# Kernel optimization log

Hardware: AMD Instinct MI355X
Metric: run time of the kernel (lower is better)

## Reference

```python
import jax, jax.numpy as jnp
import numpy as np

K = 1024       # num_embeddings
D = 64         # embedding_dim
DECAY = 0.99
COMMIT = 0.25
EPS = 1e-05


def setup_inputs() -> dict:
    key = jax.random.key(0)
    k1, k2, k3 = jax.random.split(key, 3)
    x = jax.random.normal(k1, (16, 64, 64, 64), jnp.float32)  # NCHW, C == D
    embedding_weight = jax.random.normal(k2, (K, D), jnp.float32)
    ema_weight = jax.random.normal(k3, (K, D), jnp.float32)
    ema_cluster_size = jnp.zeros((K,), jnp.float32)
    return {"x": x, "embedding_weight": embedding_weight,
            "ema_cluster_size": ema_cluster_size, "ema_weight": ema_weight}


def reference(x, embedding_weight, ema_cluster_size, ema_weight):
    # NCHW -> NHWC, flatten tokens
    xp = jnp.transpose(x, (0, 2, 3, 1))            # [B,H,W,D]
    flat = xp.reshape(-1, D)                        # [N,D]
    dists = ((flat ** 2).sum(1, keepdims=True)
             + (embedding_weight ** 2).sum(1)
             - 2.0 * flat @ embedding_weight.T)     # [N,K]
    idx = jnp.argmin(dists, axis=1)                 # [N]
    encodings = jax.nn.one_hot(idx, K, dtype=flat.dtype)  # [N,K]
    quantized = jnp.take(embedding_weight, idx, axis=0).reshape(xp.shape)
    # training-mode EMA updates (scatter-add instead of dense one-hot matmuls)
    counts = jnp.zeros((K,), flat.dtype).at[idx].add(1.0)
    new_cs = ema_cluster_size * DECAY + (1.0 - DECAY) * counts
    n = new_cs.sum()
    new_cs = (new_cs + EPS) / (n + K * EPS) * n     # Laplace smoothing
    dw = jnp.zeros((K, D), flat.dtype).at[idx].add(flat)
    new_ema_weight = ema_weight * DECAY + (1.0 - DECAY) * dw
    new_embedding = new_ema_weight / new_cs[:, None]
    # commitment loss and straight-through estimator
    e_latent_loss = jnp.mean((jax.lax.stop_gradient(quantized) - xp) ** 2)
    loss = COMMIT * e_latent_loss
    q_st = xp + jax.lax.stop_gradient(quantized - xp)
    return (loss, jnp.transpose(q_st, (0, 3, 1, 2)), encodings,
            new_embedding, new_cs, new_ema_weight)
```

## Files before the change

kernel.cpp:

```cpp
#include <hip/hip_runtime.h>

#define HW 4096
#define DECAYF 0.99f
#define ONEMF 0.01f
#define EPSF 1e-5f

typedef __bf16 bf16x8 __attribute__((ext_vector_type(8)));
typedef float f32x4 __attribute__((ext_vector_type(4)));
typedef unsigned short ushort8 __attribute__((ext_vector_type(8)));

#define WS_COUNTS 65536
#define WS_NCHALF 66560
#define WS_SSE    67584
#define WS_EHI    67600
#define WS_ELO    100368

__device__ __forceinline__ float wave_reduce_add(float v) {
#pragma unroll
    for (int o = 32; o > 0; o >>= 1) v += __shfl_xor(v, o, 64);
    return v;
}

__device__ __forceinline__ unsigned short bf_rne(float f) {
    unsigned int u = __float_as_uint(f);
    unsigned int r = u + 0x7fffu + ((u >> 16) & 1u);
    return (unsigned short)(r >> 16);
}

__global__ __launch_bounds__(256) void prep_kernel(const float* __restrict__ E,
                                                   float* __restrict__ ws) {
    const int bid = blockIdx.x, tid = threadIdx.x;
    const int id = bid * 256 + tid;
    ws[id] = 0.0f;
    if (bid < 4) ws[WS_COUNTS + bid * 256 + tid] = 0.0f;
    if (bid == 4 && tid == 0) ws[WS_SSE] = 0.0f;
    const float v = E[id];
    const unsigned short h = bf_rne(v);
    const float hf = __uint_as_float((unsigned int)h << 16);
    const unsigned short l = bf_rne(v - hf);
    ((unsigned short*)(ws + WS_EHI))[id] = h;
    ((unsigned short*)(ws + WS_ELO))[id] = l;
    const int lane = tid & 63;
    const float s = wave_reduce_add(v * v);
    if (lane == 0) ws[WS_NCHALF + (id >> 6)] = -0.5f * s;
}

__global__ __launch_bounds__(256) void vq_main(const float* __restrict__ x,
                                               const float* __restrict__ E,
                                               float* __restrict__ out,
                                               float* __restrict__ ws) {
    const int tid = threadIdx.x;
    const int lane = tid & 63;
    const int w = tid >> 6;
    const int blk = blockIdx.x;
    const int b = blk >> 5;
    const int hw0 = (blk & 31) << 7;
    const int tok0 = blk << 7;

    __shared__ float xs[128 * 68];
    __shared__ int i1sh[128], i2sh[128], idx_sh[128];

    {
        const float* xb = x + ((size_t)b << 18) + hw0;
#pragma unroll
        for (int cc = 0; cc < 32; ++cc) {
            const int id = cc * 256 + tid;
            const int c = id >> 7, t = id & 127;
            xs[t * 68 + c] = xb[((size_t)c << 12) + t];
        }
    }
    __syncthreads();

    const int q = lane >> 4, m = lane & 15;

    bf16x8 Ah[2][2], Al[2][2];
#pragma unroll
    for (int t = 0; t < 2; ++t) {
        const int tok = w * 32 + t * 16 + m;
#pragma unroll
        for (int s = 0; s < 2; ++s) {
            const float* p = &xs[tok * 68 + s * 32 + q * 8];
            ushort8 hu, lu;
#pragma unroll
            for (int j = 0; j < 8; ++j) {
                const float f = p[j];
                const unsigned short h = bf_rne(f);
                const float hf = __uint_as_float((unsigned int)h << 16);
                hu[j] = h;
                lu[j] = bf_rne(f - hf);
            }
            Ah[t][s] = __builtin_bit_cast(bf16x8, hu);
            Al[t][s] = __builtin_bit_cast(bf16x8, lu);
        }
    }

    const ushort8* __restrict__ Ehp = (const ushort8*)(ws + WS_EHI);
    const ushort8* __restrict__ Elp = (const ushort8*)(ws + WS_ELO);
    const float* __restrict__ ncp = ws + WS_NCHALF;

    float b1[2][4], b2[2][4];
    int i1[2][4], i2[2][4];
#pragma unroll
    for (int t = 0; t < 2; ++t)
#pragma unroll
        for (int r = 0; r < 4; ++r) { b1[t][r] = -1e30f; b2[t][r] = -1e30f; i1[t][r] = 0; i2[t][r] = 1; }

    ushort8 nb0h = Ehp[m * 8 + q];
    ushort8 nb1h = Ehp[m * 8 + 4 + q];
    ushort8 nb0l = Elp[m * 8 + q];
    ushort8 nb1l = Elp[m * 8 + 4 + q];
    float nnc = ncp[m];

    for (int ck = 0; ck < 64; ++ck) {
        const ushort8 c0h = nb0h, c1h = nb1h, c0l = nb0l, c1l = nb1l;
        const float nc = nnc;
        if (ck < 63) {
            const int code = (ck + 1) * 16 + m;
            nb0h = Ehp[code * 8 + q];
            nb1h = Ehp[code * 8 + 4 + q];
            nb0l = Elp[code * 8 + q];
            nb1l = Elp[code * 8 + 4 + q];
            nnc = ncp[code];
        }
        const bf16x8 bh0 = __builtin_bit_cast(bf16x8, c0h);
        const bf16x8 bh1 = __builtin_bit_cast(bf16x8, c1h);
        const bf16x8 bl0 = __builtin_bit_cast(bf16x8, c0l);
        const bf16x8 bl1 = __builtin_bit_cast(bf16x8, c1l);
        const int idx = ck * 16 + m;
#pragma unroll
        for (int t = 0; t < 2; ++t) {
            f32x4 acc = {nc, nc, nc, nc};
            acc = __builtin_amdgcn_mfma_f32_16x16x32_bf16(Ah[t][0], bh0, acc, 0, 0, 0);
            acc = __builtin_amdgcn_mfma_f32_16x16x32_bf16(Ah[t][1], bh1, acc, 0, 0, 0);
            acc = __builtin_amdgcn_mfma_f32_16x16x32_bf16(Al[t][0], bh0, acc, 0, 0, 0);
            acc = __builtin_amdgcn_mfma_f32_16x16x32_bf16(Al[t][1], bh1, acc, 0, 0, 0);
            acc = __builtin_amdgcn_mfma_f32_16x16x32_bf16(Ah[t][0], bl0, acc, 0, 0, 0);
            acc = __builtin_amdgcn_mfma_f32_16x16x32_bf16(Ah[t][1], bl1, acc, 0, 0, 0);
#pragma unroll
            for (int r = 0; r < 4; ++r) {
                const float s = acc[r];
                const bool cA = s > b1[t][r];
                const bool cB = s > b2[t][r];
                b2[t][r] = cA ? b1[t][r] : (cB ? s : b2[t][r]);
                i2[t][r] = cA ? i1[t][r] : (cB ? idx : i2[t][r]);
                b1[t][r] = cA ? s : b1[t][r];
                i1[t][r] = cA ? idx : i1[t][r];
            }
        }
    }

#pragma unroll
    for (int d = 1; d < 16; d <<= 1) {
#pragma unroll
        for (int t = 0; t < 2; ++t)
#pragma unroll
            for (int r = 0; r < 4; ++r) {
                const float ob1 = __shfl_xor(b1[t][r], d, 64);
                const int   oi1 = __shfl_xor(i1[t][r], d, 64);
                const float ob2 = __shfl_xor(b2[t][r], d, 64);
                const int   oi2 = __shfl_xor(i2[t][r], d, 64);
                const bool wv = ob1 > b1[t][r];
                const float t1 = wv ? ob1 : b1[t][r]; const int ti1 = wv ? oi1 : i1[t][r];
                const float sA = wv ? b1[t][r] : ob1; const int siA = wv ? i1[t][r] : oi1;
                const float sB = wv ? ob2 : b2[t][r]; const int siB = wv ? oi2 : i2[t][r];
                const bool w2 = sB > sA;
                b1[t][r] = t1; i1[t][r] = ti1;
                b2[t][r] = w2 ? sB : sA; i2[t][r] = w2 ? siB : siA;
            }
    }
    if (m == 0) {
#pragma unroll
        for (int t = 0; t < 2; ++t)
#pragma unroll
            for (int r = 0; r < 4; ++r) {
                const int tokL = w * 32 + t * 16 + q * 4 + r;
                i1sh[tokL] = i1[t][r];
                i2sh[tokL] = i2[t][r];
            }
    }

    float dval = 0.0f;
    if (lane < 32) {
        const int tokL = w * 32 + lane;
        const int I1 = i1sh[tokL], I2 = i2sh[tokL];
        const int ca = I1 < I2 ? I1 : I2;
        const int cb = I1 < I2 ? I2 : I1;
        const float* Ea = E + ca * 64;
        const float* Eb = E + cb * 64;
        const float* xr = &xs[tokL * 68];
        double sa = 0, ea = 0, sb = 0, eb = 0, x2 = 0;
#pragma unroll 8
        for (int c = 0; c < 64; ++c) {
            const double xv = (double)xr[c];
            const double va = (double)Ea[c], vb = (double)Eb[c];
            sa += xv * va; ea += va * va;
            sb += xv * vb; eb += vb * vb;
            x2 += xv * xv;
        }
        const double qa = ea - 2.0 * sa;
        const double qb = eb - 2.0 * sb;
        int best; double qq;
        if (qb < qa) { best = cb; qq = qb; } else { best = ca; qq = qa; }
        idx_sh[tokL] = best;
        float dd = (float)(qq + x2);
        dval = dd < 0.f ? 0.f : dd;
        atomicAdd(&ws[WS_COUNTS + best], 1.0f);
    }
    const float ssum = wave_reduce_add(dval);
    if (lane == 0) atomicAdd(&ws[WS_SSE], ssum);
    __syncthreads();

    float* outq = out + 1;
#pragma unroll
    for (int cc = 0; cc < 32; ++cc) {
        const int id = cc * 256 + tid;
        const int c = id >> 7, t = id & 127;
        const int kb = idx_sh[t];
        const float xv = xs[t * 68 + c];
        const float eq = E[kb * 64 + c];
        outq[((size_t)(b * 64 + c) << 12) + hw0 + t] = xv + (eq - xv);
    }
#pragma unroll 4
    for (int tt = 0; tt < 32; ++tt) {
        const int t = w * 32 + tt;
        const int kb = idx_sh[t];
        atomicAdd(&ws[kb * 64 + lane], xs[t * 68 + lane]);
    }
    {
        float* enc = out + 1 + (size_t)4194304;
        const int c0 = tid << 2;
        for (int t = 0; t < 128; ++t) {
            const int kb = idx_sh[t];
            f32x4 v;
            v[0] = (c0 == kb) ? 1.0f : 0.0f;
            v[1] = (c0 + 1 == kb) ? 1.0f : 0.0f;
            v[2] = (c0 + 2 == kb) ? 1.0f : 0.0f;
            v[3] = (c0 + 3 == kb) ? 1.0f : 0.0f;
            __builtin_nontemporal_store(v, (f32x4*)(enc + (size_t)(tok0 + t) * 1024 + c0));
        }
    }
}

__global__ __launch_bounds__(1024) void fin_cs(const float* __restrict__ cs_in,
                                               float* __restrict__ out,
                                               const float* __restrict__ ws) {
    __shared__ float red[16];
    __shared__ float n_sh;
    const int tid = threadIdx.x;
    const float raw = cs_in[tid] * DECAYF + ONEMF * ws[WS_COUNTS + tid];
    const float s = wave_reduce_add(raw);
    if ((tid & 63) == 0) red[tid >> 6] = s;
    __syncthreads();
    if (tid == 0) {
        float n = 0.f;
#pragma unroll
        for (int i = 0; i < 16; ++i) n += red[i];
        n_sh = n;
        out[0] = 0.25f * ws[WS_SSE] * (1.0f / 4194304.0f);
    }
    __syncthreads();
    const float n = n_sh;
    out[71368705 + tid] = (raw + EPSF) / (n + 1024.0f * EPSF) * n;
}

__global__ __launch_bounds__(256) void fin_w(const float* __restrict__ emaw,
                                             float* __restrict__ out,
                                             const float* __restrict__ ws) {
    const int i = blockIdx.x * 256 + threadIdx.x;
    const float val = emaw[i] * DECAYF + ONEMF * ws[i];
    out[71369729 + i] = val;
    const float cs = out[71368705 + (i >> 6)];
    out[71303169 + i] = val / cs;
}

extern "C" void kernel_launch(void* const* d_in, const int* in_sizes, int n_in,
                              void* d_out, int out_size, void* d_ws, size_t ws_size,
                              hipStream_t stream) {
    const float* x    = (const float*)d_in[0];
    const float* E    = (const float*)d_in[1];
    const float* cs   = (const float*)d_in[2];
    const float* emaw = (const float*)d_in[3];
    float* out = (float*)d_out;
    float* ws  = (float*)d_ws;

    prep_kernel<<<256, 256, 0, stream>>>(E, ws);
    vq_main<<<512, 256, 0, stream>>>(x, E, out, ws);
    fin_cs<<<1, 1024, 0, stream>>>(cs, out, ws);
    fin_w<<<256, 256, 0, stream>>>(emaw, out, ws);
}
```

Before: 415.7 us.

## Halve tokens per block, pack argmin keys, privatize dw atomics across 16 copies

Each block now handles 64 tokens instead of 128, doubling the grid to 1024 blocks and giving each wave one 16-token tile. The top-2 argmin tracking is replaced with packed unsigned keys: a biased score with the chunk index in the low 6 bits, kept with a max and a med3. The 16 per-lane candidates are merged through shared memory instead of shuffles. The EMA weight scatter-add goes to 16 private copies in workspace to cut atomic contention, and fin_w sums them, which adds extra zeroing and reads. Packing the index into the mantissa and the fixed bias lower score precision, which the exact fp64 re-check of the top two candidates is meant to cover.

```diff
diff --git a/kernel.cpp b/kernel.cpp
--- a/kernel.cpp
+++ b/kernel.cpp
@@ -4,16 +4,18 @@
 #define DECAYF 0.99f
 #define ONEMF 0.01f
 #define EPSF 1e-5f
+#define BIAS 192.0f
 
 typedef __bf16 bf16x8 __attribute__((ext_vector_type(8)));
 typedef float f32x4 __attribute__((ext_vector_type(4)));
 typedef unsigned short ushort8 __attribute__((ext_vector_type(8)));
 
-#define WS_COUNTS 65536
-#define WS_NCHALF 66560
-#define WS_SSE    67584
-#define WS_EHI    67600
-#define WS_ELO    100368
+#define WS_DW     0
+#define WS_COUNTS 1048576
+#define WS_NCHALF 1049600
+#define WS_SSE    1050624
+#define WS_EHI    1050640
+#define WS_ELO    1083408
 
 __device__ __forceinline__ float wave_reduce_add(float v) {
 #pragma unroll
@@ -27,22 +29,30 @@
     return (unsigned short)(r >> 16);
 }
 
+__device__ __forceinline__ unsigned med3u(unsigned a, unsigned b, unsigned c) {
+    unsigned mn = a < b ? a : b;
+    unsigned mx = a > b ? a : b;
+    unsigned t = mx < c ? mx : c;
+    return mn > t ? mn : t;
+}
+
 __global__ __launch_bounds__(256) void prep_kernel(const float* __restrict__ E,
                                                    float* __restrict__ ws) {
     const int bid = blockIdx.x, tid = threadIdx.x;
     const int id = bid * 256 + tid;
-    ws[id] = 0.0f;
+    ws[WS_DW + id] = 0.0f;
     if (bid < 4) ws[WS_COUNTS + bid * 256 + tid] = 0.0f;
     if (bid == 4 && tid == 0) ws[WS_SSE] = 0.0f;
-    const float v = E[id];
-    const unsigned short h = bf_rne(v);
-    const float hf = __uint_as_float((unsigned int)h << 16);
-    const unsigned short l = bf_rne(v - hf);
-    ((unsigned short*)(ws + WS_EHI))[id] = h;
-    ((unsigned short*)(ws + WS_ELO))[id] = l;
-    const int lane = tid & 63;
-    const float s = wave_reduce_add(v * v);
-    if (lane == 0) ws[WS_NCHALF + (id >> 6)] = -0.5f * s;
+    if (bid < 256) {
+        const float v = E[id];
+        const unsigned short h = bf_rne(v);
+        const float hf = __uint_as_float((unsigned int)h << 16);
+        const unsigned short l = bf_rne(v - hf);
+        ((unsigned short*)(ws + WS_EHI))[id] = h;
+        ((unsigned short*)(ws + WS_ELO))[id] = l;
+        const float s = wave_reduce_add(v * v);
+        if ((tid & 63) == 0) ws[WS_NCHALF + (id >> 6)] = -0.5f * s;
+    }
 }
 
 __global__ __launch_bounds__(256) void vq_main(const float* __restrict__ x,
@@ -52,31 +62,30 @@
     const int tid = threadIdx.x;
     const int lane = tid & 63;
     const int w = tid >> 6;
+    const int q = lane >> 4, m = lane & 15;
     const int blk = blockIdx.x;
-    const int b = blk >> 5;
-    const int hw0 = (blk & 31) << 7;
-    const int tok0 = blk << 7;
-
-    __shared__ float xs[128 * 68];
-    __shared__ int i1sh[128], i2sh[128], idx_sh[128];
-
-    {
-        const float* xb = x + ((size_t)b << 18) + hw0;
-#pragma unroll
-        for (int cc = 0; cc < 32; ++cc) {
+    const int bb = blk >> 6;
+    const int hw0 = (blk & 63) << 6;
+    const int tok0 = blk << 6;
+
+    __shared__ float xs[64 * 68];
+    __shared__ unsigned t1s[4][16][16], t2s[4][16][16];
+    __shared__ int idx_sh[64];
+
+    {
+        const float* xb = x + ((size_t)bb << 18) + hw0;
+#pragma unroll
+        for (int cc = 0; cc < 16; ++cc) {
             const int id = cc * 256 + tid;
-            const int c = id >> 7, t = id & 127;
+            const int c = id >> 6, t = id & 63;
             xs[t * 68 + c] = xb[((size_t)c << 12) + t];
         }
     }
     __syncthreads();
 
-    const int q = lane >> 4, m = lane & 15;
-
-    bf16x8 Ah[2][2], Al[2][2];
-#pragma unroll
-    for (int t = 0; t < 2; ++t) {
-        const int tok = w * 32 + t * 16 + m;
+    bf16x8 Ah[2], Al[2];
+    {
+        const int tok = w * 16 + m;
 #pragma unroll
         for (int s = 0; s < 2; ++s) {
             const float* p = &xs[tok * 68 + s * 32 + q * 8];
@@ -89,8 +98,8 @@
                 hu[j] = h;
                 lu[j] = bf_rne(f - hf);
             }
-            Ah[t][s] = __builtin_bit_cast(bf16x8, hu);
-            Al[t][s] = __builtin_bit_cast(bf16x8, lu);
+            Ah[s] = __builtin_bit_cast(bf16x8, hu);
+            Al[s] = __builtin_bit_cast(bf16x8, lu);
         }
     }
 
@@ -98,12 +107,7 @@
     const ushort8* __restrict__ Elp = (const ushort8*)(ws + WS_ELO);
     const float* __restrict__ ncp = ws + WS_NCHALF;
 
-    float b1[2][4], b2[2][4];
-    int i1[2][4], i2[2][4];
-#pragma unroll
-    for (int t = 0; t < 2; ++t)
-#pragma unroll
-        for (int r = 0; r < 4; ++r) { b1[t][r] = -1e30f; b2[t][r] = -1e30f; i1[t][r] = 0; i2[t][r] = 1; }
+    unsigned b1[4] = {0, 0, 0, 0}, b2[4] = {0, 0, 0, 0};
 
     ushort8 nb0h = Ehp[m * 8 + q];
     ushort8 nb1h = Ehp[m * 8 + 4 + q];
@@ -126,65 +130,46 @@
         const bf16x8 bh1 = __builtin_bit_cast(bf16x8, c1h);
         const bf16x8 bl0 = __builtin_bit_cast(bf16x8, c0l);
         const bf16x8 bl1 = __builtin_bit_cast(bf16x8, c1l);
-        const int idx = ck * 16 + m;
-#pragma unroll
-        for (int t = 0; t < 2; ++t) {
-            f32x4 acc = {nc, nc, nc, nc};
-            acc = __builtin_amdgcn_mfma_f32_16x16x32_bf16(Ah[t][0], bh0, acc, 0, 0, 0);
-            acc = __builtin_amdgcn_mfma_f32_16x16x32_bf16(Ah[t][1], bh1, acc, 0, 0, 0);
-            acc = __builtin_amdgcn_mfma_f32_16x16x32_bf16(Al[t][0], bh0, acc, 0, 0, 0);
-            acc = __builtin_amdgcn_mfma_f32_16x16x32_bf16(Al[t][1], bh1, acc, 0, 0, 0);
-            acc = __builtin_amdgcn_mfma_f32_16x16x32_bf16(Ah[t][0], bl0, acc, 0, 0, 0);
-            acc = __builtin_amdgcn_mfma_f32_16x16x32_bf16(Ah[t][1], bl1, acc, 0, 0, 0);
-#pragma unroll
-            for (int r = 0; r < 4; ++r) {
-                const float s = acc[r];
-                const bool cA = s > b1[t][r];
-                const bool cB = s > b2[t][r];
-                b2[t][r] = cA ? b1[t][r] : (cB ? s : b2[t][r]);
-                i2[t][r] = cA ? i1[t][r] : (cB ? idx : i2[t][r]);
-                b1[t][r] = cA ? s : b1[t][r];
-                i1[t][r] = cA ? idx : i1[t][r];
-            }
-        }
-    }
-
-#pragma unroll
-    for (int d = 1; d < 16; d <<= 1) {
-#pragma unroll
-        for (int t = 0; t < 2; ++t)
-#pragma unroll
-            for (int r = 0; r < 4; ++r) {
-                const float ob1 = __shfl_xor(b1[t][r], d, 64);
-                const int   oi1 = __shfl_xor(i1[t][r], d, 64);
-                const float ob2 = __shfl_xor(b2[t][r], d, 64);
-                const int   oi2 = __shfl_xor(i2[t][r], d, 64);
-                const bool wv = ob1 > b1[t][r];
-                const float t1 = wv ? ob1 : b1[t][r]; const int ti1 = wv ? oi1 : i1[t][r];
-                const float sA = wv ? b1[t][r] : ob1; const int siA = wv ? i1[t][r] : oi1;
-                const float sB = wv ? ob2 : b2[t][r]; const int siB = wv ? oi2 : i2[t][r];
-                const bool w2 = sB > sA;
-                b1[t][r] = t1; i1[t][r] = ti1;
-                b2[t][r] = w2 ? sB : sA; i2[t][r] = w2 ? siB : siA;
-            }
-    }
-    if (m == 0) {
-#pragma unroll
-        for (int t = 0; t < 2; ++t)
-#pragma unroll
-            for (int r = 0; r < 4; ++r) {
-                const int tokL = w * 32 + t * 16 + q * 4 + r;
-                i1sh[tokL] = i1[t][r];
-                i2sh[tokL] = i2[t][r];
-            }
+        const float base = nc + BIAS;
+        f32x4 acc_a = {base, base, base, base};
+        f32x4 acc_b = {0.f, 0.f, 0.f, 0.f};
+        acc_a = __builtin_amdgcn_mfma_f32_16x16x32_bf16(Ah[0], bh0, acc_a, 0, 0, 0);
+        acc_b = __builtin_amdgcn_mfma_f32_16x16x32_bf16(Ah[1], bh1, acc_b, 0, 0, 0);
+        acc_a = __builtin_amdgcn_mfma_f32_16x16x32_bf16(Al[0], bh0, acc_a, 0, 0, 0);
+        acc_b = __builtin_amdgcn_mfma_f32_16x16x32_bf16(Al[1], bh1, acc_b, 0, 0, 0);
+        acc_a = __builtin_amdgcn_mfma_f32_16x16x32_bf16(Ah[0], bl0, acc_a, 0, 0, 0);
+        acc_b = __builtin_amdgcn_mfma_f32_16x16x32_bf16(Ah[1], bl1, acc_b, 0, 0, 0);
+#pragma unroll
+        for (int r = 0; r < 4; ++r) {
+            const float s = acc_a[r] + acc_b[r];
+            const unsigned p = (__float_as_uint(s) & ~63u) | (unsigned)ck;
+            b2[r] = med3u(b1[r], b2[r], p);
+            b1[r] = b1[r] > p ? b1[r] : p;
+        }
+    }
+
+#pragma unroll
+    for (int r = 0; r < 4; ++r) {
+        t1s[w][q * 4 + r][m] = b1[r];
+        t2s[w][q * 4 + r][m] = b2[r];
     }
 
     float dval = 0.0f;
-    if (lane < 32) {
-        const int tokL = w * 32 + lane;
-        const int I1 = i1sh[tokL], I2 = i2sh[tokL];
-        const int ca = I1 < I2 ? I1 : I2;
-        const int cb = I1 < I2 ? I2 : I1;
+    if (lane < 16) {
+        unsigned s1 = 0, s2 = 0;
+        int c1 = 0, c2 = 0;
+#pragma unroll 4
+        for (int mm = 0; mm < 16; ++mm) {
+            const unsigned a = t1s[w][lane][mm];
+            const int codeA = (int)((a & 63u) << 4) | mm;
+            if (a > s1) { s2 = s1; c2 = c1; s1 = a; c1 = codeA; }
+            else if (a > s2) { s2 = a; c2 = codeA; }
+            const unsigned bsec = t2s[w][lane][mm];
+            if (bsec > s2) { s2 = bsec; c2 = (int)((bsec & 63u) << 4) | mm; }
+        }
+        const int tokL = w * 16 + lane;
+        const int ca = c1 < c2 ? c1 : c2;
+        const int cb = c1 < c2 ? c2 : c1;
         const float* Ea = E + ca * 64;
         const float* Eb = E + cb * 64;
         const float* xr = &xs[tokL * 68];
@@ -212,24 +197,27 @@
 
     float* outq = out + 1;
 #pragma unroll
-    for (int cc = 0; cc < 32; ++cc) {
+    for (int cc = 0; cc < 16; ++cc) {
         const int id = cc * 256 + tid;
-        const int c = id >> 7, t = id & 127;
+        const int c = id >> 6, t = id & 63;
         const int kb = idx_sh[t];
         const float xv = xs[t * 68 + c];
         const float eq = E[kb * 64 + c];
-        outq[((size_t)(b * 64 + c) << 12) + hw0 + t] = xv + (eq - xv);
-    }
+        outq[((size_t)(bb * 64 + c) << 12) + hw0 + t] = xv + (eq - xv);
+    }
+    {
+        float* dwr = ws + WS_DW + (size_t)(blk & 15) * 65536;
 #pragma unroll 4
-    for (int tt = 0; tt < 32; ++tt) {
-        const int t = w * 32 + tt;
-        const int kb = idx_sh[t];
-        atomicAdd(&ws[kb * 64 + lane], xs[t * 68 + lane]);
+        for (int tt = 0; tt < 16; ++tt) {
+            const int t = w * 16 + tt;
+            const int kb = idx_sh[t];
+            atomicAdd(&dwr[kb * 64 + lane], xs[t * 68 + lane]);
+        }
     }
     {
         float* enc = out + 1 + (size_t)4194304;
         const int c0 = tid << 2;
-        for (int t = 0; t < 128; ++t) {
+        for (int t = 0; t < 64; ++t) {
             const int kb = idx_sh[t];
             f32x4 v;
             v[0] = (c0 == kb) ? 1.0f : 0.0f;
@@ -267,7 +255,10 @@
                                              float* __restrict__ out,
                                              const float* __restrict__ ws) {
     const int i = blockIdx.x * 256 + threadIdx.x;
-    const float val = emaw[i] * DECAYF + ONEMF * ws[i];
+    float acc = 0.f;
+#pragma unroll
+    for (int p = 0; p < 16; ++p) acc += ws[WS_DW + p * 65536 + i];
+    const float val = emaw[i] * DECAYF + ONEMF * acc;
     out[71369729 + i] = val;
     const float cs = out[71368705 + (i >> 6)];
     out[71303169 + i] = val / cs;
@@ -283,8 +274,8 @@
     float* out = (float*)d_out;
     float* ws  = (float*)d_ws;
 
-    prep_kernel<<<256, 256, 0, stream>>>(E, ws);
-    vq_main<<<512, 256, 0, stream>>>(x, E, out, ws);
+    prep_kernel<<<4096, 256, 0, stream>>>(E, ws);
+    vq_main<<<1024, 256, 0, stream>>>(x, E, out, ws);
     fin_cs<<<1, 1024, 0, stream>>>(cs, out, ws);
     fin_w<<<256, 256, 0, stream>>>(emaw, out, ws);
 }
```

Result: slower. 462.9 us (+11.3%).
